# Kernel optimization log

Measured on AMD Instinct MI355X. Metric: run time of the kernel, lower is better.

## Reference

```python
import jax, jax.numpy as jnp
import numpy as np

IN, H = 24, 128


def _lstm_last(x, W_ih, W_hh, b_ih, b_hh):
    # x: [B, T, IN]. PyTorch gate order: i, f, g, o. Returns final hidden state [B, H].
    B = x.shape[0]
    b = b_ih + b_hh  # [4H]
    # Precompute input projections for all timesteps: [T, B, 4H]
    xg = jnp.einsum('bti,gi->tbg', x, W_ih) + b

    def step(carry, xg_t):
        h, c = carry
        gates = xg_t + h @ W_hh.T  # [B, 4H]
        i, f, g, o = jnp.split(gates, 4, axis=-1)
        i = jax.nn.sigmoid(i)
        f = jax.nn.sigmoid(f)
        g = jnp.tanh(g)
        o = jax.nn.sigmoid(o)
        c = f * c + i * g
        h = o * jnp.tanh(c)
        return (h, c), None

    h0 = jnp.zeros((B, H), x.dtype)
    (h, _), _ = jax.lax.scan(step, (h0, h0), xg)
    return h


def setup_inputs() -> dict:
    key = jax.random.key(0)
    ks = jax.random.split(key, 10)
    s_ih = 1.0 / np.sqrt(H)
    return {
        'x': jax.random.normal(ks[0], (1024, 512, IN), jnp.float32),
        'additional_input': jax.random.normal(ks[1], (1024, 2), jnp.float32),
        'W_ih': jax.random.uniform(ks[2], (4 * H, IN), jnp.float32, -s_ih, s_ih),
        'W_hh': jax.random.uniform(ks[3], (4 * H, H), jnp.float32, -s_ih, s_ih),
        'b_ih': jax.random.uniform(ks[4], (4 * H,), jnp.float32, -s_ih, s_ih),
        'b_hh': jax.random.uniform(ks[5], (4 * H,), jnp.float32, -s_ih, s_ih),
        'W1': jax.random.uniform(ks[6], (64, H + 2), jnp.float32, -1/np.sqrt(H + 2), 1/np.sqrt(H + 2)),
        'b1': jax.random.uniform(ks[7], (64,), jnp.float32, -1/np.sqrt(H + 2), 1/np.sqrt(H + 2)),
        'W2': jax.random.uniform(ks[8], (3, 64), jnp.float32, -1/8.0, 1/8.0),
        'b2': jax.random.uniform(ks[9], (3,), jnp.float32, -1/8.0, 1/8.0),
    }


def reference(x, additional_input, W_ih, W_hh, b_ih, b_hh, W1, b1, W2, b2):
    h_last = _lstm_last(x, W_ih, W_hh, b_ih, b_hh)  # [B, H]
    combined = jnp.concatenate([h_last, additional_input], axis=1)  # [B, H+2]
    # fc: Dropout (identity in eval) -> ReLU -> Linear -> Dropout -> ReLU -> Linear
    z = jax.nn.relu(combined) @ W1.T + b1
    out = jax.nn.relu(z) @ W2.T + b2  # [B, 3]
    return out
```

## Files before the change

### kernel.cpp

```cpp
#include <hip/hip_runtime.h>
#include <cstdint>
#include <cstddef>

#define TSTEPS 512
#define INP    24
#define HID    128
#define BB     4
#define NKT    5
#define VSTR   168

typedef __attribute__((ext_vector_type(8))) _Float16 half8;
typedef __attribute__((ext_vector_type(4))) float f32x4;

__device__ __forceinline__ float rcp_f(float v) { return __builtin_amdgcn_rcpf(v); }
__device__ __forceinline__ float sigm_f(float v) {
    return rcp_f(1.0f + __expf(-v));
}
__device__ __forceinline__ float tanh_f(float v) {
    return 1.0f - 2.0f * rcp_f(1.0f + __expf(2.0f * v));
}
__device__ __forceinline__ unsigned pack2h(float a, float b) {
    union { _Float16 h[2]; unsigned u; } z;
    z.h[0] = (_Float16)a; z.h[1] = (_Float16)b;
    return z.u;
}
__device__ __forceinline__ float sel4(const f32x4 a, bool rb0, bool rb1) {
    const float lo = rb0 ? a[1] : a[0];
    const float hi = rb0 ? a[3] : a[2];
    return rb1 ? hi : lo;
}

__global__ __launch_bounds__(512)
void lstm_fused(
    const float* __restrict__ x,
    const float* __restrict__ addin,
    const float* __restrict__ W_ih,
    const float* __restrict__ W_hh,
    const float* __restrict__ b_ih,
    const float* __restrict__ b_hh,
    const float* __restrict__ W1,
    const float* __restrict__ b1,
    const float* __restrict__ W2,
    const float* __restrict__ b2,
    float* __restrict__ out)
{
    __shared__ _Float16 v_s[2][BB * VSTR];
    __shared__ float z_s[BB][64];

    const int t    = threadIdx.x;
    const int lane = t & 63;
    const int wv   = t >> 6;
    const int ncol = lane & 15;
    const int quad = lane >> 4;
    const int b0   = blockIdx.x * BB;
    const int bsel = ncol & 3;
    const bool rb0 = (ncol >> 2) & 1;
    const bool rb1 = (ncol >> 3) & 1;

    half8 A_w[4][NKT];
    #pragma unroll
    for (int g = 0; g < 4; ++g) {
        const int row = g * HID + wv * 16 + ncol;
        #pragma unroll
        for (int kt = 0; kt < NKT; ++kt) {
            half8 frag;
            #pragma unroll
            for (int j = 0; j < 8; ++j) {
                const int k = kt * 32 + quad * 8 + j;
                float w = 0.0f;
                if (k < HID)            w = W_hh[row * HID + k];
                else if (k < HID + INP) w = W_ih[row * INP + (k - HID)];
                frag[j] = (_Float16)w;
            }
            A_w[g][kt] = frag;
        }
    }

    f32x4 biasv[4];
    #pragma unroll
    for (int g = 0; g < 4; ++g) {
        #pragma unroll
        for (int r = 0; r < 4; ++r) {
            const int u = wv * 16 + quad * 4 + r;
            biasv[g][r] = b_ih[g * HID + u] + b_hh[g * HID + u];
        }
    }

    const int uj = wv * 16 + quad * 4 + (ncol >> 2);
    float c_reg = 0.0f;

    const int sb = t / 12;
    const int kk = t - sb * 12;
    const size_t xrow = (size_t)(b0 + sb) * TSTEPS;

    for (int i = t; i < BB * VSTR; i += 512) {
        v_s[0][i] = (_Float16)0.0f; v_s[1][i] = (_Float16)0.0f;
    }
    __syncthreads();
    if (t < 48) {
        const float2 x0 = *(const float2*)(x + (xrow + 0) * INP + kk * 2);
        const float2 x1 = *(const float2*)(x + (xrow + 1) * INP + kk * 2);
        *(unsigned*)&v_s[0][sb * VSTR + HID + kk * 2] = pack2h(x0.x, x0.y);
        *(unsigned*)&v_s[1][sb * VSTR + HID + kk * 2] = pack2h(x1.x, x1.y);
    }
    float2 xq = {0.f, 0.f};
    if (t < 48) {
        xq = *(const float2*)(x + (xrow + 2) * INP + kk * 2);
    }
    __syncthreads();

    f32x4 aci, acf, acg, aco;
    {
        const half8 bx = *(const half8*)(&v_s[0][0] + bsel * VSTR + HID + quad * 8);
        aci = __builtin_amdgcn_mfma_f32_16x16x32_f16(A_w[0][4], bx, biasv[0], 0, 0, 0);
        acf = __builtin_amdgcn_mfma_f32_16x16x32_f16(A_w[1][4], bx, biasv[1], 0, 0, 0);
        acg = __builtin_amdgcn_mfma_f32_16x16x32_f16(A_w[2][4], bx, biasv[2], 0, 0, 0);
        aco = __builtin_amdgcn_mfma_f32_16x16x32_f16(A_w[3][4], bx, biasv[3], 0, 0, 0);
    }
    __syncthreads();

    #pragma unroll 2
    for (int ts = 0; ts < TSTEPS; ++ts) {
        const int pb = ts & 1, nb = pb ^ 1;

        float2 xn = {0.f, 0.f};
        if (t < 48) {
            const int tsn = (ts + 3 < TSTEPS) ? ts + 3 : TSTEPS - 1;
            xn = *(const float2*)(x + (xrow + tsn) * INP + kk * 2);
            *(unsigned*)&v_s[pb][sb * VSTR + HID + kk * 2] = pack2h(xq.x, xq.y);
        }

        const half8 bx = *(const half8*)(&v_s[nb][0] + bsel * VSTR + HID + quad * 8);

        const _Float16* vh = v_s[pb];
        f32x4 ai = aci, af = acf, ag = acg, ao = aco;
        #pragma unroll
        for (int kt = 0; kt < 4; ++kt) {
            const half8 bh = *(const half8*)(vh + bsel * VSTR + kt * 32 + quad * 8);
            ai = __builtin_amdgcn_mfma_f32_16x16x32_f16(A_w[0][kt], bh, ai, 0, 0, 0);
            af = __builtin_amdgcn_mfma_f32_16x16x32_f16(A_w[1][kt], bh, af, 0, 0, 0);
            ag = __builtin_amdgcn_mfma_f32_16x16x32_f16(A_w[2][kt], bh, ag, 0, 0, 0);
            ao = __builtin_amdgcn_mfma_f32_16x16x32_f16(A_w[3][kt], bh, ao, 0, 0, 0);
        }

        const float si = sel4(ai, rb0, rb1);
        const float sf = sel4(af, rb0, rb1);
        const float sg = sel4(ag, rb0, rb1);
        const float so = sel4(ao, rb0, rb1);

        aci = __builtin_amdgcn_mfma_f32_16x16x32_f16(A_w[0][4], bx, biasv[0], 0, 0, 0);
        acf = __builtin_amdgcn_mfma_f32_16x16x32_f16(A_w[1][4], bx, biasv[1], 0, 0, 0);
        acg = __builtin_amdgcn_mfma_f32_16x16x32_f16(A_w[2][4], bx, biasv[2], 0, 0, 0);
        aco = __builtin_amdgcn_mfma_f32_16x16x32_f16(A_w[3][4], bx, biasv[3], 0, 0, 0);

        {
            const float gi = sigm_f(si);
            const float gf = sigm_f(sf);
            const float gg = tanh_f(sg);
            const float go = sigm_f(so);
            c_reg = gf * c_reg + gi * gg;
            const float h = go * tanh_f(c_reg);
            v_s[nb][bsel * VSTR + uj] = (_Float16)h;
        }

        if (t < 48) xq = xn;

        __syncthreads();
    }

    if (t < 64 * BB) {
        const int b = t >> 6, u = t & 63;
        const float* w = W1 + u * 130;
        float a = b1[u];
        #pragma unroll 16
        for (int k = 0; k < HID; ++k) {
            const float hv = (float)v_s[0][b * VSTR + k];
            a += fmaxf(hv, 0.0f) * w[k];
        }
        const float a0 = addin[(size_t)(b0 + b) * 2 + 0];
        const float a1 = addin[(size_t)(b0 + b) * 2 + 1];
        a += fmaxf(a0, 0.0f) * w[128] + fmaxf(a1, 0.0f) * w[129];
        z_s[b][u] = fmaxf(a, 0.0f);
    }
    __syncthreads();
    if (t < 3 * BB) {
        const int b = t / 3, o = t - 3 * b;
        const float* w = W2 + o * 64;
        float a = b2[o];
        #pragma unroll
        for (int k = 0; k < 64; ++k)
            a += z_s[b][k] * w[k];
        out[(size_t)(b0 + b) * 3 + o] = a;
    }
}

extern "C" void kernel_launch(void* const* d_in, const int* in_sizes, int n_in,
                              void* d_out, int out_size, void* d_ws, size_t ws_size,
                              hipStream_t stream) {
    const float* x     = (const float*)d_in[0];
    const float* addin = (const float*)d_in[1];
    const float* W_ih  = (const float*)d_in[2];
    const float* W_hh  = (const float*)d_in[3];
    const float* b_ih  = (const float*)d_in[4];
    const float* b_hh  = (const float*)d_in[5];
    const float* W1    = (const float*)d_in[6];
    const float* b1    = (const float*)d_in[7];
    const float* W2    = (const float*)d_in[8];
    const float* b2    = (const float*)d_in[9];
    float* outp        = (float*)d_out;

    const int B = in_sizes[0] / (TSTEPS * INP);
    const int grid = B / BB;

    lstm_fused<<<grid, 512, 0, stream>>>(x, addin, W_ih, W_hh, b_ih, b_hh,
                                         W1, b1, W2, b2, outp);
}
```

Measured before the change: 403.3 us.

## Add dedicated staging wavefront for x prefetch, hoist h-fragment LDS loads

```diff
diff --git a/kernel.cpp b/kernel.cpp
--- a/kernel.cpp
+++ b/kernel.cpp
@@ -8,6 +8,7 @@
 #define BB     4
 #define NKT    5
 #define VSTR   168
+#define NTHR   576
 
 typedef __attribute__((ext_vector_type(8))) _Float16 half8;
 typedef __attribute__((ext_vector_type(4))) float f32x4;
@@ -30,7 +31,7 @@
     return rb1 ? hi : lo;
 }
 
-__global__ __launch_bounds__(512)
+__global__ __launch_bounds__(NTHR)
 void lstm_fused(
     const float* __restrict__ x,
     const float* __restrict__ addin,
@@ -50,6 +51,8 @@
     const int t    = threadIdx.x;
     const int lane = t & 63;
     const int wv   = t >> 6;
+    const bool is_stage = (wv == 8);
+    const int wvc  = is_stage ? 0 : wv;
     const int ncol = lane & 15;
     const int quad = lane >> 4;
     const int b0   = blockIdx.x * BB;
@@ -60,7 +63,7 @@
     half8 A_w[4][NKT];
     #pragma unroll
     for (int g = 0; g < 4; ++g) {
-        const int row = g * HID + wv * 16 + ncol;
+        const int row = g * HID + wvc * 16 + ncol;
         #pragma unroll
         for (int kt = 0; kt < NKT; ++kt) {
             half8 frag;
@@ -81,91 +84,107 @@
     for (int g = 0; g < 4; ++g) {
         #pragma unroll
         for (int r = 0; r < 4; ++r) {
-            const int u = wv * 16 + quad * 4 + r;
+            const int u = wvc * 16 + quad * 4 + r;
             biasv[g][r] = b_ih[g * HID + u] + b_hh[g * HID + u];
         }
     }
 
-    const int uj = wv * 16 + quad * 4 + (ncol >> 2);
+    const int uj = wvc * 16 + quad * 4 + (ncol >> 2);
     float c_reg = 0.0f;
 
-    const int sb = t / 12;
-    const int kk = t - sb * 12;
-    const size_t xrow = (size_t)(b0 + sb) * TSTEPS;
-
-    for (int i = t; i < BB * VSTR; i += 512) {
+    const int sb = lane / 12;
+    const int kk = lane - sb * 12;
+    const size_t xrow = (size_t)(b0 + (sb & 3)) * TSTEPS;
+
+    for (int i = t; i < BB * VSTR; i += NTHR) {
         v_s[0][i] = (_Float16)0.0f; v_s[1][i] = (_Float16)0.0f;
     }
     __syncthreads();
-    if (t < 48) {
-        const float2 x0 = *(const float2*)(x + (xrow + 0) * INP + kk * 2);
-        const float2 x1 = *(const float2*)(x + (xrow + 1) * INP + kk * 2);
-        *(unsigned*)&v_s[0][sb * VSTR + HID + kk * 2] = pack2h(x0.x, x0.y);
-        *(unsigned*)&v_s[1][sb * VSTR + HID + kk * 2] = pack2h(x1.x, x1.y);
-    }
-    float2 xq = {0.f, 0.f};
-    if (t < 48) {
-        xq = *(const float2*)(x + (xrow + 2) * INP + kk * 2);
-    }
-    __syncthreads();
-
-    f32x4 aci, acf, acg, aco;
-    {
-        const half8 bx = *(const half8*)(&v_s[0][0] + bsel * VSTR + HID + quad * 8);
-        aci = __builtin_amdgcn_mfma_f32_16x16x32_f16(A_w[0][4], bx, biasv[0], 0, 0, 0);
-        acf = __builtin_amdgcn_mfma_f32_16x16x32_f16(A_w[1][4], bx, biasv[1], 0, 0, 0);
-        acg = __builtin_amdgcn_mfma_f32_16x16x32_f16(A_w[2][4], bx, biasv[2], 0, 0, 0);
-        aco = __builtin_amdgcn_mfma_f32_16x16x32_f16(A_w[3][4], bx, biasv[3], 0, 0, 0);
-    }
-    __syncthreads();
-
-    #pragma unroll 2
-    for (int ts = 0; ts < TSTEPS; ++ts) {
-        const int pb = ts & 1, nb = pb ^ 1;
-
-        float2 xn = {0.f, 0.f};
-        if (t < 48) {
-            const int tsn = (ts + 3 < TSTEPS) ? ts + 3 : TSTEPS - 1;
-            xn = *(const float2*)(x + (xrow + tsn) * INP + kk * 2);
-            *(unsigned*)&v_s[pb][sb * VSTR + HID + kk * 2] = pack2h(xq.x, xq.y);
-        }
-
-        const half8 bx = *(const half8*)(&v_s[nb][0] + bsel * VSTR + HID + quad * 8);
-
-        const _Float16* vh = v_s[pb];
-        f32x4 ai = aci, af = acf, ag = acg, ao = aco;
-        #pragma unroll
-        for (int kt = 0; kt < 4; ++kt) {
-            const half8 bh = *(const half8*)(vh + bsel * VSTR + kt * 32 + quad * 8);
-            ai = __builtin_amdgcn_mfma_f32_16x16x32_f16(A_w[0][kt], bh, ai, 0, 0, 0);
-            af = __builtin_amdgcn_mfma_f32_16x16x32_f16(A_w[1][kt], bh, af, 0, 0, 0);
-            ag = __builtin_amdgcn_mfma_f32_16x16x32_f16(A_w[2][kt], bh, ag, 0, 0, 0);
-            ao = __builtin_amdgcn_mfma_f32_16x16x32_f16(A_w[3][kt], bh, ao, 0, 0, 0);
-        }
-
-        const float si = sel4(ai, rb0, rb1);
-        const float sf = sel4(af, rb0, rb1);
-        const float sg = sel4(ag, rb0, rb1);
-        const float so = sel4(ao, rb0, rb1);
-
-        aci = __builtin_amdgcn_mfma_f32_16x16x32_f16(A_w[0][4], bx, biasv[0], 0, 0, 0);
-        acf = __builtin_amdgcn_mfma_f32_16x16x32_f16(A_w[1][4], bx, biasv[1], 0, 0, 0);
-        acg = __builtin_amdgcn_mfma_f32_16x16x32_f16(A_w[2][4], bx, biasv[2], 0, 0, 0);
-        aco = __builtin_amdgcn_mfma_f32_16x16x32_f16(A_w[3][4], bx, biasv[3], 0, 0, 0);
-
+
+    if (is_stage) {
+        float2 xq = {0.f, 0.f};
+        if (lane < 48) {
+            const float2 x0 = *(const float2*)(x + (xrow + 0) * INP + kk * 2);
+            const float2 x1 = *(const float2*)(x + (xrow + 1) * INP + kk * 2);
+            *(unsigned*)&v_s[0][sb * VSTR + HID + kk * 2] = pack2h(x0.x, x0.y);
+            *(unsigned*)&v_s[1][sb * VSTR + HID + kk * 2] = pack2h(x1.x, x1.y);
+            xq = *(const float2*)(x + (xrow + 2) * INP + kk * 2);
+        }
+        __syncthreads();
+        __syncthreads();
+        for (int ts = 0; ts < TSTEPS; ++ts) {
+            const int pb = ts & 1;
+            if (lane < 48) {
+                const int tsn = (ts + 3 < TSTEPS) ? ts + 3 : TSTEPS - 1;
+                const float2 xn = *(const float2*)(x + (xrow + tsn) * INP + kk * 2);
+                *(unsigned*)&v_s[pb][sb * VSTR + HID + kk * 2] = pack2h(xq.x, xq.y);
+                xq = xn;
+            }
+            __syncthreads();
+        }
+    } else {
+        __syncthreads();
+
+        f32x4 aci, acf, acg, aco;
         {
-            const float gi = sigm_f(si);
-            const float gf = sigm_f(sf);
-            const float gg = tanh_f(sg);
-            const float go = sigm_f(so);
-            c_reg = gf * c_reg + gi * gg;
-            const float h = go * tanh_f(c_reg);
-            v_s[nb][bsel * VSTR + uj] = (_Float16)h;
-        }
-
-        if (t < 48) xq = xn;
-
-        __syncthreads();
+            const half8 bx = *(const half8*)(&v_s[0][0] + bsel * VSTR + HID + quad * 8);
+            aci = __builtin_amdgcn_mfma_f32_16x16x32_f16(A_w[0][4], bx, biasv[0], 0, 0, 0);
+            acf = __builtin_amdgcn_mfma_f32_16x16x32_f16(A_w[1][4], bx, biasv[1], 0, 0, 0);
+            acg = __builtin_amdgcn_mfma_f32_16x16x32_f16(A_w[2][4], bx, biasv[2], 0, 0, 0);
+            aco = __builtin_amdgcn_mfma_f32_16x16x32_f16(A_w[3][4], bx, biasv[3], 0, 0, 0);
+        }
+        __syncthreads();
+
+        #pragma unroll 2
+        for (int ts = 0; ts < TSTEPS; ++ts) {
+            const int pb = ts & 1, nb = pb ^ 1;
+            const _Float16* vh = v_s[pb];
+
+            const half8 bh0 = *(const half8*)(vh + bsel * VSTR + 0 * 32 + quad * 8);
+            const half8 bh1 = *(const half8*)(vh + bsel * VSTR + 1 * 32 + quad * 8);
+            const half8 bh2 = *(const half8*)(vh + bsel * VSTR + 2 * 32 + quad * 8);
+            const half8 bh3 = *(const half8*)(vh + bsel * VSTR + 3 * 32 + quad * 8);
+            const half8 bx  = *(const half8*)(&v_s[nb][0] + bsel * VSTR + HID + quad * 8);
+
+            f32x4 ai = __builtin_amdgcn_mfma_f32_16x16x32_f16(A_w[0][0], bh0, aci, 0, 0, 0);
+            f32x4 af = __builtin_amdgcn_mfma_f32_16x16x32_f16(A_w[1][0], bh0, acf, 0, 0, 0);
+            f32x4 ag = __builtin_amdgcn_mfma_f32_16x16x32_f16(A_w[2][0], bh0, acg, 0, 0, 0);
+            f32x4 ao = __builtin_amdgcn_mfma_f32_16x16x32_f16(A_w[3][0], bh0, aco, 0, 0, 0);
+            ai = __builtin_amdgcn_mfma_f32_16x16x32_f16(A_w[0][1], bh1, ai, 0, 0, 0);
+            af = __builtin_amdgcn_mfma_f32_16x16x32_f16(A_w[1][1], bh1, af, 0, 0, 0);
+            ag = __builtin_amdgcn_mfma_f32_16x16x32_f16(A_w[2][1], bh1, ag, 0, 0, 0);
+            ao = __builtin_amdgcn_mfma_f32_16x16x32_f16(A_w[3][1], bh1, ao, 0, 0, 0);
+            ai = __builtin_amdgcn_mfma_f32_16x16x32_f16(A_w[0][2], bh2, ai, 0, 0, 0);
+            af = __builtin_amdgcn_mfma_f32_16x16x32_f16(A_w[1][2], bh2, af, 0, 0, 0);
+            ag = __builtin_amdgcn_mfma_f32_16x16x32_f16(A_w[2][2], bh2, ag, 0, 0, 0);
+            ao = __builtin_amdgcn_mfma_f32_16x16x32_f16(A_w[3][2], bh2, ao, 0, 0, 0);
+            ai = __builtin_amdgcn_mfma_f32_16x16x32_f16(A_w[0][3], bh3, ai, 0, 0, 0);
+            af = __builtin_amdgcn_mfma_f32_16x16x32_f16(A_w[1][3], bh3, af, 0, 0, 0);
+            ag = __builtin_amdgcn_mfma_f32_16x16x32_f16(A_w[2][3], bh3, ag, 0, 0, 0);
+            ao = __builtin_amdgcn_mfma_f32_16x16x32_f16(A_w[3][3], bh3, ao, 0, 0, 0);
+
+            const float si = sel4(ai, rb0, rb1);
+            const float sf = sel4(af, rb0, rb1);
+            const float sg = sel4(ag, rb0, rb1);
+            const float so = sel4(ao, rb0, rb1);
+
+            aci = __builtin_amdgcn_mfma_f32_16x16x32_f16(A_w[0][4], bx, biasv[0], 0, 0, 0);
+            acf = __builtin_amdgcn_mfma_f32_16x16x32_f16(A_w[1][4], bx, biasv[1], 0, 0, 0);
+            acg = __builtin_amdgcn_mfma_f32_16x16x32_f16(A_w[2][4], bx, biasv[2], 0, 0, 0);
+            aco = __builtin_amdgcn_mfma_f32_16x16x32_f16(A_w[3][4], bx, biasv[3], 0, 0, 0);
+
+            {
+                const float gi = sigm_f(si);
+                const float gf = sigm_f(sf);
+                const float gg = tanh_f(sg);
+                const float go = sigm_f(so);
+                c_reg = gf * c_reg + gi * gg;
+                const float h = go * tanh_f(c_reg);
+                v_s[nb][bsel * VSTR + uj] = (_Float16)h;
+            }
+
+            __syncthreads();
+        }
     }
 
     if (t < 64 * BB) {
@@ -212,6 +231,6 @@
     const int B = in_sizes[0] / (TSTEPS * INP);
     const int grid = B / BB;
 
-    lstm_fused<<<grid, 512, 0, stream>>>(x, addin, W_ih, W_hh, b_ih, b_hh,
-                                         W1, b1, W2, b2, outp);
-}
+    lstm_fused<<<grid, NTHR, 0, stream>>>(x, addin, W_ih, W_hh, b_ih, b_hh,
+                                          W1, b1, W2, b2, outp);
+}
```

Measured after the change: 373.6 us. 1.08x faster.

## Halve block to four waves, each computing two 16-unit hidden tiles

Applied to the files above, without the earlier changes.

```diff
diff --git a/kernel.cpp b/kernel.cpp
--- a/kernel.cpp
+++ b/kernel.cpp
@@ -8,6 +8,7 @@
 #define BB     4
 #define NKT    5
 #define VSTR   168
+#define NTHR   256
 
 typedef __attribute__((ext_vector_type(8))) _Float16 half8;
 typedef __attribute__((ext_vector_type(4))) float f32x4;
@@ -30,7 +31,7 @@
     return rb1 ? hi : lo;
 }
 
-__global__ __launch_bounds__(512)
+__global__ __launch_bounds__(NTHR) __attribute__((amdgpu_waves_per_eu(1, 1)))
 void lstm_fused(
     const float* __restrict__ x,
     const float* __restrict__ addin,
@@ -57,65 +58,71 @@
     const bool rb0 = (ncol >> 2) & 1;
     const bool rb1 = (ncol >> 3) & 1;
 
-    half8 A_w[4][NKT];
+    half8 A_w[2][4][NKT];
     #pragma unroll
-    for (int g = 0; g < 4; ++g) {
-        const int row = g * HID + wv * 16 + ncol;
-        #pragma unroll
-        for (int kt = 0; kt < NKT; ++kt) {
-            half8 frag;
-            #pragma unroll
-            for (int j = 0; j < 8; ++j) {
-                const int k = kt * 32 + quad * 8 + j;
-                float w = 0.0f;
-                if (k < HID)            w = W_hh[row * HID + k];
-                else if (k < HID + INP) w = W_ih[row * INP + (k - HID)];
-                frag[j] = (_Float16)w;
+    for (int m = 0; m < 2; ++m) {
+        #pragma unroll
+        for (int g = 0; g < 4; ++g) {
+            const int row = g * HID + wv * 32 + m * 16 + ncol;
+            #pragma unroll
+            for (int kt = 0; kt < NKT; ++kt) {
+                half8 frag;
+                #pragma unroll
+                for (int j = 0; j < 8; ++j) {
+                    const int k = kt * 32 + quad * 8 + j;
+                    float w = 0.0f;
+                    if (k < HID)            w = W_hh[row * HID + k];
+                    else if (k < HID + INP) w = W_ih[row * INP + (k - HID)];
+                    frag[j] = (_Float16)w;
+                }
+                A_w[m][g][kt] = frag;
             }
-            A_w[g][kt] = frag;
-        }
-    }
-
-    f32x4 biasv[4];
+        }
+    }
+
+    f32x4 biasv[2][4];
     #pragma unroll
-    for (int g = 0; g < 4; ++g) {
-        #pragma unroll
-        for (int r = 0; r < 4; ++r) {
-            const int u = wv * 16 + quad * 4 + r;
-            biasv[g][r] = b_ih[g * HID + u] + b_hh[g * HID + u];
-        }
-    }
-
-    const int uj = wv * 16 + quad * 4 + (ncol >> 2);
-    float c_reg = 0.0f;
-
-    const int sb = t / 12;
-    const int kk = t - sb * 12;
-    const size_t xrow = (size_t)(b0 + sb) * TSTEPS;
-
-    for (int i = t; i < BB * VSTR; i += 512) {
+    for (int m = 0; m < 2; ++m) {
+        #pragma unroll
+        for (int g = 0; g < 4; ++g) {
+            #pragma unroll
+            for (int r = 0; r < 4; ++r) {
+                const int u = wv * 32 + m * 16 + quad * 4 + r;
+                biasv[m][g][r] = b_ih[g * HID + u] + b_hh[g * HID + u];
+            }
+        }
+    }
+
+    const int uj0 = wv * 32 + quad * 4 + (ncol >> 2);
+    float creg[2] = {0.f, 0.f};
+
+    const int kk = lane;
+    const size_t xrow = (size_t)(b0 + wv) * TSTEPS;
+
+    for (int i = t; i < BB * VSTR; i += NTHR) {
         v_s[0][i] = (_Float16)0.0f; v_s[1][i] = (_Float16)0.0f;
     }
     __syncthreads();
-    if (t < 48) {
+
+    float2 xq = {0.f, 0.f};
+    if (lane < 12) {
         const float2 x0 = *(const float2*)(x + (xrow + 0) * INP + kk * 2);
         const float2 x1 = *(const float2*)(x + (xrow + 1) * INP + kk * 2);
-        *(unsigned*)&v_s[0][sb * VSTR + HID + kk * 2] = pack2h(x0.x, x0.y);
-        *(unsigned*)&v_s[1][sb * VSTR + HID + kk * 2] = pack2h(x1.x, x1.y);
-    }
-    float2 xq = {0.f, 0.f};
-    if (t < 48) {
+        *(unsigned*)&v_s[0][wv * VSTR + HID + kk * 2] = pack2h(x0.x, x0.y);
+        *(unsigned*)&v_s[1][wv * VSTR + HID + kk * 2] = pack2h(x1.x, x1.y);
         xq = *(const float2*)(x + (xrow + 2) * INP + kk * 2);
     }
     __syncthreads();
 
-    f32x4 aci, acf, acg, aco;
+    f32x4 ac[2][4];
     {
-        const half8 bx = *(const half8*)(&v_s[0][0] + bsel * VSTR + HID + quad * 8);
-        aci = __builtin_amdgcn_mfma_f32_16x16x32_f16(A_w[0][4], bx, biasv[0], 0, 0, 0);
-        acf = __builtin_amdgcn_mfma_f32_16x16x32_f16(A_w[1][4], bx, biasv[1], 0, 0, 0);
-        acg = __builtin_amdgcn_mfma_f32_16x16x32_f16(A_w[2][4], bx, biasv[2], 0, 0, 0);
-        aco = __builtin_amdgcn_mfma_f32_16x16x32_f16(A_w[3][4], bx, biasv[3], 0, 0, 0);
+        const half8 bx0 = *(const half8*)(&v_s[0][0] + bsel * VSTR + HID + quad * 8);
+        #pragma unroll
+        for (int m = 0; m < 2; ++m)
+            #pragma unroll
+            for (int g = 0; g < 4; ++g)
+                ac[m][g] = __builtin_amdgcn_mfma_f32_16x16x32_f16(
+                    A_w[m][g][4], bx0, biasv[m][g], 0, 0, 0);
     }
     __syncthreads();
 
@@ -124,51 +131,66 @@
         const int pb = ts & 1, nb = pb ^ 1;
 
         float2 xn = {0.f, 0.f};
-        if (t < 48) {
+        if (lane < 12) {
             const int tsn = (ts + 3 < TSTEPS) ? ts + 3 : TSTEPS - 1;
             xn = *(const float2*)(x + (xrow + tsn) * INP + kk * 2);
-            *(unsigned*)&v_s[pb][sb * VSTR + HID + kk * 2] = pack2h(xq.x, xq.y);
-        }
-
+            *(unsigned*)&v_s[pb][wv * VSTR + HID + kk * 2] = pack2h(xq.x, xq.y);
+        }
+
+        const _Float16* vh = v_s[pb];
+        half8 bh[4];
+        #pragma unroll
+        for (int kt = 0; kt < 4; ++kt)
+            bh[kt] = *(const half8*)(vh + bsel * VSTR + kt * 32 + quad * 8);
         const half8 bx = *(const half8*)(&v_s[nb][0] + bsel * VSTR + HID + quad * 8);
 
-        const _Float16* vh = v_s[pb];
-        f32x4 ai = aci, af = acf, ag = acg, ao = aco;
-        #pragma unroll
-        for (int kt = 0; kt < 4; ++kt) {
-            const half8 bh = *(const half8*)(vh + bsel * VSTR + kt * 32 + quad * 8);
-            ai = __builtin_amdgcn_mfma_f32_16x16x32_f16(A_w[0][kt], bh, ai, 0, 0, 0);
-            af = __builtin_amdgcn_mfma_f32_16x16x32_f16(A_w[1][kt], bh, af, 0, 0, 0);
-            ag = __builtin_amdgcn_mfma_f32_16x16x32_f16(A_w[2][kt], bh, ag, 0, 0, 0);
-            ao = __builtin_amdgcn_mfma_f32_16x16x32_f16(A_w[3][kt], bh, ao, 0, 0, 0);
-        }
-
-        const float si = sel4(ai, rb0, rb1);
-        const float sf = sel4(af, rb0, rb1);
-        const float sg = sel4(ag, rb0, rb1);
-        const float so = sel4(ao, rb0, rb1);
-
-        aci = __builtin_amdgcn_mfma_f32_16x16x32_f16(A_w[0][4], bx, biasv[0], 0, 0, 0);
-        acf = __builtin_amdgcn_mfma_f32_16x16x32_f16(A_w[1][4], bx, biasv[1], 0, 0, 0);
-        acg = __builtin_amdgcn_mfma_f32_16x16x32_f16(A_w[2][4], bx, biasv[2], 0, 0, 0);
-        aco = __builtin_amdgcn_mfma_f32_16x16x32_f16(A_w[3][4], bx, biasv[3], 0, 0, 0);
-
-        {
-            const float gi = sigm_f(si);
-            const float gf = sigm_f(sf);
-            const float gg = tanh_f(sg);
-            const float go = sigm_f(so);
-            c_reg = gf * c_reg + gi * gg;
-            const float h = go * tanh_f(c_reg);
-            v_s[nb][bsel * VSTR + uj] = (_Float16)h;
-        }
-
-        if (t < 48) xq = xn;
+        f32x4 a[2][4];
+        #pragma unroll
+        for (int m = 0; m < 2; ++m)
+            #pragma unroll
+            for (int g = 0; g < 4; ++g)
+                a[m][g] = __builtin_amdgcn_mfma_f32_16x16x32_f16(
+                    A_w[m][g][0], bh[0], ac[m][g], 0, 0, 0);
+        #pragma unroll
+        for (int kt = 1; kt < 4; ++kt)
+            #pragma unroll
+            for (int m = 0; m < 2; ++m)
+                #pragma unroll
+                for (int g = 0; g < 4; ++g)
+                    a[m][g] = __builtin_amdgcn_mfma_f32_16x16x32_f16(
+                        A_w[m][g][kt], bh[kt], a[m][g], 0, 0, 0);
+
+        float s[2][4];
+        #pragma unroll
+        for (int m = 0; m < 2; ++m)
+            #pragma unroll
+            for (int g = 0; g < 4; ++g)
+                s[m][g] = sel4(a[m][g], rb0, rb1);
+
+        #pragma unroll
+        for (int m = 0; m < 2; ++m)
+            #pragma unroll
+            for (int g = 0; g < 4; ++g)
+                ac[m][g] = __builtin_amdgcn_mfma_f32_16x16x32_f16(
+                    A_w[m][g][4], bx, biasv[m][g], 0, 0, 0);
+
+        #pragma unroll
+        for (int m = 0; m < 2; ++m) {
+            const float gi = sigm_f(s[m][0]);
+            const float gf = sigm_f(s[m][1]);
+            const float gg = tanh_f(s[m][2]);
+            const float go = sigm_f(s[m][3]);
+            creg[m] = gf * creg[m] + gi * gg;
+            const float h = go * tanh_f(creg[m]);
+            v_s[nb][bsel * VSTR + uj0 + m * 16] = (_Float16)h;
+        }
+
+        if (lane < 12) xq = xn;
 
         __syncthreads();
     }
 
-    if (t < 64 * BB) {
+    {
         const int b = t >> 6, u = t & 63;
         const float* w = W1 + u * 130;
         float a = b1[u];
@@ -212,6 +234,6 @@
     const int B = in_sizes[0] / (TSTEPS * INP);
     const int grid = B / BB;
 
-    lstm_fused<<<grid, 512, 0, stream>>>(x, addin, W_ih, W_hh, b_ih, b_hh,
-                                         W1, b1, W2, b2, outp);
-}
+    lstm_fused<<<grid, NTHR, 0, stream>>>(x, addin, W_ih, W_hh, b_ih, b_hh,
+                                          W1, b1, W2, b2, outp);
+}
```

Measured after the change: 541.3 us. 1.34x slower.
